# Kernel optimization log

Hardware: AMD Instinct MI355X
Metric: run time of the kernel (lower is better)

Reference implementation:

```python
import jax, jax.numpy as jnp
import numpy as np

B, N, C = 1, 768, 128


def _safe_cdist(x):
    # Euclidean pairwise distance, grad-safe at zero (diagonal).
    sq = jnp.sum(x * x, axis=-1)  # (b, n)
    d2 = sq[:, :, None] + sq[:, None, :] - 2.0 * jnp.einsum('bmi,bni->bmn', x, x)
    d2 = jnp.maximum(d2, 0.0)
    pos = d2 > 0
    return jnp.where(pos, jnp.sqrt(jnp.where(pos, d2, 1.0)), 0.0)


def _bilinear(h, Wa, ba, Wb, bb):
    # Gated bilinear unit: Linear_a(h) * Linear_b(h)
    return (h @ Wa.T + ba) * (h @ Wb.T + bb)


def setup_inputs() -> dict:
    key = jax.random.key(0)
    ks = jax.random.split(key, 16)
    x = jax.random.normal(ks[0], (B, N, 3), dtype=jnp.float32)

    def lin(k, fan_in, fan_out):
        k1, k2 = jax.random.split(k)
        s = 1.0 / np.sqrt(fan_in)
        W = jax.random.uniform(k1, (fan_out, fan_in), jnp.float32, -s, s)
        b = jax.random.uniform(k2, (fan_out,), jnp.float32, -s, s)
        return W, b

    Wa1, ba1 = lin(ks[1], 3, C)
    Wb1, bb1 = lin(ks[2], 3, C)
    Wa2, ba2 = lin(ks[3], C, C)
    Wb2, bb2 = lin(ks[4], C, C)
    Wa3, ba3 = lin(ks[5], C, C)
    Wb3, bb3 = lin(ks[6], C, C)
    Wf, _ = lin(ks[7], C, 2)  # final bias unused by the einsum in forward
    return {"x": x,
            "Wa1": Wa1, "ba1": ba1, "Wb1": Wb1, "bb1": bb1,
            "Wa2": Wa2, "ba2": ba2, "Wb2": Wb2, "bb2": bb2,
            "Wa3": Wa3, "ba3": ba3, "Wb3": Wb3, "bb3": bb3,
            "Wf": Wf}


def reference(x, Wa1, ba1, Wb1, bb1, Wa2, ba2, Wb2, bb2, Wa3, ba3, Wb3, bb3, Wf):
    b, n, _ = x.shape
    nrm = jnp.linalg.norm(x, axis=-1, keepdims=True)          # (b, n, 1)
    nrm_m = jnp.broadcast_to(nrm, (b, n, n))                  # row norms
    d = _safe_cdist(x)                                        # (b, n, n)
    h = jnp.stack([d, nrm_m, jnp.swapaxes(nrm_m, 1, 2)], axis=-1)  # (b,n,n,3)
    h = _bilinear(h, Wa1, ba1, Wb1, bb1)
    h = _bilinear(h, Wa2, ba2, Wb2, bb2)
    h = _bilinear(h, Wa3, ba3, Wb3, bb3)                      # (b,n,n,C)
    att = jax.nn.softmax(h, axis=-2)                          # softmax over n (dim=-2)
    # einsum('bmnc,bni->bmic') followed by sum over m, fused:
    agg = jnp.einsum('bmnc,bni->bic', att, x)                 # (b, 3, C)
    agg = jnp.swapaxes(agg, 1, 2)                             # (b, C, 3)
    out = jnp.einsum('bnd,on->bod', agg, Wf)                  # (b, 2, 3)
    return jnp.concatenate([x[:, :1], out[:, :2]], axis=1)    # (b, 3, 3)
```

## Files before the change

### kernel.cpp

```cpp
#include <hip/hip_runtime.h>

#define NPTS 768
#define CCH  128
#define NM4  36
#define NM2  10
#define TILE 128
#define NCHUNK 6
#define PAIR (NPTS*CCH)
#define NACC 384
#define FINB 96
#define LOG2E 1.4426950408889634f
#define NQW  (NPTS*8*CCH)

typedef __attribute__((ext_vector_type(8))) short bf16x8;
typedef __attribute__((ext_vector_type(16))) float f32x16;
union Frag { unsigned int u[4]; bf16x8 h; };

__device__ __forceinline__ float fast_exp2(float x) {
  return __builtin_amdgcn_exp2f(x);
}

__device__ __forceinline__ void split3(float x, unsigned int& h0,
                                       unsigned int& h1, unsigned int& h2) {
  const unsigned int b0 = __float_as_uint(x);
  h0 = b0 >> 16;
  const float r1 = x - __uint_as_float(b0 & 0xFFFF0000u);
  const unsigned int b1 = __float_as_uint(r1);
  h1 = b1 >> 16;
  const float r2 = r1 - __uint_as_float(b1 & 0xFFFF0000u);
  h2 = __float_as_uint(r2) >> 16;
}

__device__ __forceinline__ int t4i(int a, int b, int c) {
  int t = 0;
  for (int aa = 0; aa < a; ++aa) t += (5 - aa) * (6 - aa) / 2;
  for (int bb = 0; bb < b; ++bb) t += (5 - a - bb);
  return t + c;
}
__device__ __forceinline__ int t2i(int a, int b, int c) {
  int t = 0;
  for (int aa = 0; aa < a; ++aa) t += (3 - aa) * (4 - aa) / 2;
  for (int bb = 0; bb < b; ++bb) t += (3 - a - bb);
  return t + c;
}

__global__ __launch_bounds__(128) void k_fold12(
    const float* __restrict__ x,
    const float* __restrict__ Wa1, const float* __restrict__ ba1,
    const float* __restrict__ Wb1, const float* __restrict__ bb1,
    const float* __restrict__ Wa2, const float* __restrict__ ba2,
    const float* __restrict__ Wb2, const float* __restrict__ bb2,
    float* __restrict__ norms, float* __restrict__ C2m,
    float* __restrict__ apart, unsigned int* __restrict__ ticket) {
  __shared__ float sA[128][NM2];
  __shared__ float sB[128][NM2];
  const int c = blockIdx.x;
  const int k = threadIdx.x;

  if (c < 6) {
    const int i = c*128 + k;
    const float p0 = x[3*i], p1 = x[3*i+1], p2 = x[3*i+2];
    norms[i] = sqrtf(p0*p0 + p1*p1 + p2*p2);
  }
  if (c == 6) {
    apart[k] = 0.f; apart[CCH + k] = 0.f; apart[2*CCH + k] = 0.f;
    if (k == 0) *ticket = 0u;
  }

  {
    const float A0 = Wa1[3*k], A1 = Wa1[3*k+1], A2c = Wa1[3*k+2], A3 = ba1[k];
    const float B0 = Wb1[3*k], B1 = Wb1[3*k+1], B2c = Wb1[3*k+2], B3 = bb1[k];
    const float g0 = A3*B3;
    const float g1 = A2c*B3 + A3*B2c;
    const float g2 = A2c*B2c;
    const float g3 = A1*B3 + A3*B1;
    const float g4 = A1*B2c + A2c*B1;
    const float g5 = A1*B1;
    const float g6 = A0*B3 + A3*B0;
    const float g7 = A0*B2c + A2c*B0;
    const float g8 = A0*B1 + A1*B0;
    const float g9 = A0*B0;
    const float wa = Wa2[c*CCH + k];
    const float wb = Wb2[c*CCH + k];
    sA[k][0] = wa*g0; sB[k][0] = wb*g0;
    sA[k][1] = wa*g1; sB[k][1] = wb*g1;
    sA[k][2] = wa*g2; sB[k][2] = wb*g2;
    sA[k][3] = wa*g3; sB[k][3] = wb*g3;
    sA[k][4] = wa*g4; sB[k][4] = wb*g4;
    sA[k][5] = wa*g5; sB[k][5] = wb*g5;
    sA[k][6] = wa*g6; sB[k][6] = wb*g6;
    sA[k][7] = wa*g7; sB[k][7] = wb*g7;
    sA[k][8] = wa*g8; sB[k][8] = wb*g8;
    sA[k][9] = wa*g9; sB[k][9] = wb*g9;
  }
  __syncthreads();

  for (int s = 64; s >= 1; s >>= 1) {
    if (k < s) {
      for (int t = 0; t < NM2; ++t) {
        sA[k][t] += sA[k+s][t];
        sB[k][t] += sB[k+s][t];
      }
    }
    __syncthreads();
  }
  if (k == 0) {
    sA[0][0] += ba2[c];
    sB[0][0] += bb2[c];
  }
  __syncthreads();

  if (k < 35) {
    int rem = k, a = 0;
    while (rem >= (5 - a)*(6 - a)/2) { rem -= (5 - a)*(6 - a)/2; ++a; }
    int b = 0;
    while (rem >= 5 - a - b) { rem -= 5 - a - b; ++b; }
    const int cc = rem;
    float s = 0.f;
    const int deg = a + b + cc;
    for (int a1 = 0; a1 <= a && a1 <= 2; ++a1)
      for (int b1 = 0; b1 <= b && b1 <= 2; ++b1)
        for (int c1 = 0; c1 <= cc && c1 <= 2; ++c1) {
          const int d1 = a1 + b1 + c1;
          if (d1 <= 2 && (deg - d1) <= 2)
            s += sA[0][t2i(a1, b1, c1)]
               * sB[0][t2i(a - a1, b - b1, cc - c1)];
        }
    C2m[c*NM4 + k] = s;
  }
  if (k == 35) C2m[c*NM4 + 35] = 0.f;
}

__global__ void k_pre2(const float* __restrict__ Wa3, const float* __restrict__ ba3,
                       const float* __restrict__ Wb3, const float* __restrict__ bb3,
                       const float* __restrict__ C2m,
                       float* __restrict__ A3mT, float* __restrict__ B3mT) {
  const int c = blockIdx.x;
  const int j = threadIdx.x;
  if (j >= NM4) return;
  float sa = 0.f, sb = 0.f;
  if (j < 35) {
    for (int k = 0; k < CCH; ++k) {
      const float v = C2m[k*NM4 + j];
      sa += Wa3[c*CCH + k] * v;
      sb += Wb3[c*CCH + k] * v;
    }
    if (j == 0) { sa += ba3[c]; sb += bb3[c]; }
  }
  A3mT[j*CCH + c] = sa;
  B3mT[j*CCH + c] = sb;
}

__global__ __launch_bounds__(256) void k_pre3(
    const float* __restrict__ norms,
    const float* __restrict__ A3mT, const float* __restrict__ B3mT,
    unsigned int* __restrict__ WA0, unsigned int* __restrict__ WA1,
    unsigned int* __restrict__ WA2, unsigned int* __restrict__ WB0,
    unsigned int* __restrict__ WB1, unsigned int* __restrict__ WB2) {
  const int m = blockIdx.x;
  const float u = norms[m];
  float upow[5];
  upow[0] = 1.f; upow[1] = u; upow[2] = u*u;
  upow[3] = upow[2]*u; upow[4] = upow[2]*upow[2];

  for (int p = threadIdx.x; p < 8*CCH; p += 256) {
    const int q = p >> 7;
    const int c = p & 127;
    unsigned int wa0 = 0, wa1 = 0, wa2 = 0, wb0 = 0, wb1 = 0, wb2 = 0;
    #pragma unroll
    for (int half = 0; half < 2; ++half) {
      const int t = 2*q + half;
      int rem = t, i = 0;
      while (i < 5 && rem >= 5 - i) { rem -= 5 - i; ++i; }
      const int j = rem;
      float sa = 0.f, sb = 0.f;
      #pragma unroll
      for (int b = 0; b < 5; ++b) {
        if (i <= 4 && i + j + b <= 4) {
          const int idx = t4i(i, b, j)*CCH + c;
          sa = fmaf(A3mT[idx], upow[b], sa);
          sb = fmaf(B3mT[idx], upow[b], sb);
        }
      }
      sa *= LOG2E;
      unsigned int a0, a1, a2, b0, b1, b2;
      split3(sa, a0, a1, a2);
      split3(sb, b0, b1, b2);
      const int sh = half*16;
      wa0 |= a0 << sh; wa1 |= a1 << sh; wa2 |= a2 << sh;
      wb0 |= b0 << sh; wb1 |= b1 << sh; wb2 |= b2 << sh;
    }
    const int o = (m*8 + q)*CCH + c;
    WA0[o] = wa0; WA1[o] = wa1; WA2[o] = wa2;
    WB0[o] = wb0; WB1[o] = wb1; WB2[o] = wb2;
  }
}

__global__ __launch_bounds__(256, 2) void k_main(
    const float* __restrict__ x, const float* __restrict__ norms,
    const unsigned int* __restrict__ WA0, const unsigned int* __restrict__ WA1,
    const unsigned int* __restrict__ WA2, const unsigned int* __restrict__ WB0,
    const unsigned int* __restrict__ WB1, const unsigned int* __restrict__ WB2,
    float* __restrict__ Mp, float* __restrict__ Sp,
    float* __restrict__ A0p, float* __restrict__ A1p, float* __restrict__ A2p) {
  __shared__ __align__(16) float4 xt[TILE];
  const int tid = threadIdx.x;
  const int wid = tid >> 6;
  const int lane = tid & 63;
  const int hl = lane >> 5;
  const int ln = lane & 31;
  const int m = blockIdx.x*4 + wid;
  const int chunk = blockIdx.y;

  if (tid < TILE) {
    const int n = chunk*TILE + tid;
    xt[tid] = make_float4(x[3*n], x[3*n+1], x[3*n+2], norms[n]);
  }

  const float u = norms[m];
  const float xm0 = x[3*m], xm1 = x[3*m+1], xm2 = x[3*m+2];
  const float uu = u*u;

  Frag BA0[4], BA1[4], BA2[4], BB0[4], BB1[4], BB2[4];
  #pragma unroll
  for (int ct = 0; ct < 4; ++ct) {
    #pragma unroll
    for (int p = 0; p < 4; ++p) {
      const int o = (m*8 + hl*4 + p)*CCH + ct*32 + ln;
      BA0[ct].u[p] = WA0[o]; BA1[ct].u[p] = WA1[o]; BA2[ct].u[p] = WA2[o];
      BB0[ct].u[p] = WB0[o]; BB1[ct].u[p] = WB1[o]; BB2[ct].u[p] = WB2[o];
    }
  }

  float mrun[4], srun[4], a0r[4], a1r[4], a2r[4];
  #pragma unroll
  for (int ct = 0; ct < 4; ++ct) {
    mrun[ct] = -INFINITY; srun[ct] = 0.f;
    a0r[ct] = 0.f; a1r[ct] = 0.f; a2r[ct] = 0.f;
  }

  __syncthreads();

  for (int tile = 0; tile < 4; ++tile) {
    const float4 xn = xt[tile*32 + ln];
    const float v = xn.w;
    const float dot = xm0*xn.x + xm1*xn.y + xm2*xn.z;
    const float d2 = uu + v*v - 2.f*dot;
    const float d = (d2 > 0.f) ? sqrtf(d2) : 0.f;
    const float v2 = v*v, v3 = v2*v, v4 = v2*v2;
    const float dd = d*d, d3 = dd*d, d4 = dd*dd;
    float mono[8];
    if (hl == 0) {
      mono[0] = 1.f;   mono[1] = v;     mono[2] = v2;    mono[3] = v3;
      mono[4] = v4;    mono[5] = d;     mono[6] = d*v;   mono[7] = d*v2;
    } else {
      mono[0] = d*v3;  mono[1] = dd;    mono[2] = dd*v;  mono[3] = dd*v2;
      mono[4] = d3;    mono[5] = d3*v;  mono[6] = d4;    mono[7] = 0.f;
    }
    Frag A0f, A1f, A2f;
    #pragma unroll
    for (int p = 0; p < 4; ++p) {
      unsigned int l0, l1, l2, g0, g1, g2;
      split3(mono[2*p],   l0, l1, l2);
      split3(mono[2*p+1], g0, g1, g2);
      A0f.u[p] = l0 | (g0 << 16);
      A1f.u[p] = l1 | (g1 << 16);
      A2f.u[p] = l2 | (g2 << 16);
    }

    #pragma unroll
    for (int ct = 0; ct < 4; ++ct) {
      f32x16 accA, accB;
      #pragma unroll
      for (int r = 0; r < 16; ++r) { accA[r] = 0.f; accB[r] = 0.f; }
      accA = __builtin_amdgcn_mfma_f32_32x32x16_bf16(A2f.h, BA0[ct].h, accA, 0, 0, 0);
      accA = __builtin_amdgcn_mfma_f32_32x32x16_bf16(A1f.h, BA1[ct].h, accA, 0, 0, 0);
      accA = __builtin_amdgcn_mfma_f32_32x32x16_bf16(A0f.h, BA2[ct].h, accA, 0, 0, 0);
      accA = __builtin_amdgcn_mfma_f32_32x32x16_bf16(A1f.h, BA0[ct].h, accA, 0, 0, 0);
      accA = __builtin_amdgcn_mfma_f32_32x32x16_bf16(A0f.h, BA1[ct].h, accA, 0, 0, 0);
      accA = __builtin_amdgcn_mfma_f32_32x32x16_bf16(A0f.h, BA0[ct].h, accA, 0, 0, 0);
      accB = __builtin_amdgcn_mfma_f32_32x32x16_bf16(A2f.h, BB0[ct].h, accB, 0, 0, 0);
      accB = __builtin_amdgcn_mfma_f32_32x32x16_bf16(A1f.h, BB1[ct].h, accB, 0, 0, 0);
      accB = __builtin_amdgcn_mfma_f32_32x32x16_bf16(A0f.h, BB2[ct].h, accB, 0, 0, 0);
      accB = __builtin_amdgcn_mfma_f32_32x32x16_bf16(A1f.h, BB0[ct].h, accB, 0, 0, 0);
      accB = __builtin_amdgcn_mfma_f32_32x32x16_bf16(A0f.h, BB1[ct].h, accB, 0, 0, 0);
      accB = __builtin_amdgcn_mfma_f32_32x32x16_bf16(A0f.h, BB0[ct].h, accB, 0, 0, 0);

      float hv[16];
      #pragma unroll
      for (int r = 0; r < 16; ++r) hv[r] = accA[r]*accB[r];
      float hx = hv[0];
      #pragma unroll
      for (int r = 1; r < 16; ++r) hx = fmaxf(hx, hv[r]);
      const float mnew = fmaxf(mrun[ct], hx);
      const float sc = fast_exp2(mrun[ct] - mnew);
      mrun[ct] = mnew;
      float s_ = srun[ct]*sc, A0_ = a0r[ct]*sc, A1_ = a1r[ct]*sc, A2_ = a2r[ct]*sc;
      #pragma unroll
      for (int rg = 0; rg < 4; ++rg) {
        #pragma unroll
        for (int q = 0; q < 4; ++q) {
          const float e = fast_exp2(hv[rg*4 + q] - mnew);
          const float4 xv = xt[tile*32 + rg*8 + hl*4 + q];
          s_ += e;
          A0_ = fmaf(e, xv.x, A0_);
          A1_ = fmaf(e, xv.y, A1_);
          A2_ = fmaf(e, xv.z, A2_);
        }
      }
      srun[ct] = s_; a0r[ct] = A0_; a1r[ct] = A1_; a2r[ct] = A2_;
    }
  }

  #pragma unroll
  for (int ct = 0; ct < 4; ++ct) {
    const float om = __shfl_xor(mrun[ct], 32);
    const float os = __shfl_xor(srun[ct], 32);
    const float o0 = __shfl_xor(a0r[ct], 32);
    const float o1 = __shfl_xor(a1r[ct], 32);
    const float o2 = __shfl_xor(a2r[ct], 32);
    const float M  = fmaxf(mrun[ct], om);
    const float e1 = fast_exp2(mrun[ct] - M);
    const float e2 = fast_exp2(om - M);
    if (hl == 0) {
      const int idx = chunk*PAIR + m*CCH + ct*32 + ln;
      Mp[idx]  = M;
      Sp[idx]  = fmaf(srun[ct], e1, os*e2);
      A0p[idx] = fmaf(a0r[ct], e1, o0*e2);
      A1p[idx] = fmaf(a1r[ct], e1, o1*e2);
      A2p[idx] = fmaf(a2r[ct], e1, o2*e2);
    }
  }
}

__global__ __launch_bounds__(256) void k_fin(
    const float* __restrict__ x,
    const float* __restrict__ Mp, const float* __restrict__ Sp,
    const float* __restrict__ A0p, const float* __restrict__ A1p,
    const float* __restrict__ A2p,
    const float* __restrict__ Wf,
    float* __restrict__ apart, unsigned int* __restrict__ ticket,
    float* __restrict__ out) {
  __shared__ float red2[2][3][CCH];
  __shared__ float red[CCH][6];
  __shared__ bool last;
  const int tid = threadIdx.x;
  const int ml = tid >> 7;
  const int c = tid & 127;

  float s0 = 0.f, s1 = 0.f, s2 = 0.f;
  #pragma unroll
  for (int j = 0; j < 4; ++j) {
    const int m = blockIdx.x*8 + ml*4 + j;
    const int gid = m*CCH + c;
    float m0 = Mp[0*PAIR + gid], m1 = Mp[1*PAIR + gid], m2 = Mp[2*PAIR + gid];
    float m3 = Mp[3*PAIR + gid], m4 = Mp[4*PAIR + gid], m5 = Mp[5*PAIR + gid];
    float M = fmaxf(fmaxf(fmaxf(m0, m1), fmaxf(m2, m3)), fmaxf(m4, m5));
    float W = 0.f, g0 = 0.f, g1 = 0.f, g2 = 0.f;
    {
      const float e0 = fast_exp2(m0 - M), e1 = fast_exp2(m1 - M);
      const float e2 = fast_exp2(m2 - M), e3 = fast_exp2(m3 - M);
      const float e4 = fast_exp2(m4 - M), e5 = fast_exp2(m5 - M);
      W = Sp[0*PAIR+gid]*e0 + Sp[1*PAIR+gid]*e1 + Sp[2*PAIR+gid]*e2
        + Sp[3*PAIR+gid]*e3 + Sp[4*PAIR+gid]*e4 + Sp[5*PAIR+gid]*e5;
      g0 = A0p[0*PAIR+gid]*e0 + A0p[1*PAIR+gid]*e1 + A0p[2*PAIR+gid]*e2
         + A0p[3*PAIR+gid]*e3 + A0p[4*PAIR+gid]*e4 + A0p[5*PAIR+gid]*e5;
      g1 = A1p[0*PAIR+gid]*e0 + A1p[1*PAIR+gid]*e1 + A1p[2*PAIR+gid]*e2
         + A1p[3*PAIR+gid]*e3 + A1p[4*PAIR+gid]*e4 + A1p[5*PAIR+gid]*e5;
      g2 = A2p[0*PAIR+gid]*e0 + A2p[1*PAIR+gid]*e1 + A2p[2*PAIR+gid]*e2
         + A2p[3*PAIR+gid]*e3 + A2p[4*PAIR+gid]*e4 + A2p[5*PAIR+gid]*e5;
    }
    const float inv = 1.f / W;
    s0 = fmaf(g0, inv, s0);
    s1 = fmaf(g1, inv, s1);
    s2 = fmaf(g2, inv, s2);
  }
  red2[ml][0][c] = s0; red2[ml][1][c] = s1; red2[ml][2][c] = s2;
  __syncthreads();
  for (int p = tid; p < NACC; p += 256) {
    const int i = p >> 7, cc = p & 127;
    atomicAdd(&apart[p], red2[0][i][cc] + red2[1][i][cc]);
  }
  __threadfence();
  __syncthreads();
  if (tid == 0) {
    const unsigned int old = atomicAdd(ticket, 1u);
    last = (old == FINB - 1);
  }
  __syncthreads();
  if (!last) return;
  __threadfence();

  if (tid < CCH) {
    const int cc = tid;
    const float a0 = __hip_atomic_load(&apart[cc],          __ATOMIC_RELAXED, __HIP_MEMORY_SCOPE_AGENT);
    const float a1 = __hip_atomic_load(&apart[CCH + cc],    __ATOMIC_RELAXED, __HIP_MEMORY_SCOPE_AGENT);
    const float a2 = __hip_atomic_load(&apart[2*CCH + cc],  __ATOMIC_RELAXED, __HIP_MEMORY_SCOPE_AGENT);
    const float w0 = Wf[cc], w1 = Wf[CCH + cc];
    red[cc][0] = w0*a0; red[cc][1] = w0*a1; red[cc][2] = w0*a2;
    red[cc][3] = w1*a0; red[cc][4] = w1*a1; red[cc][5] = w1*a2;
  }
  __syncthreads();
  if (tid < 6) {
    float s = 0.f;
    for (int k = 0; k < CCH; ++k) s += red[k][tid];
    out[3 + tid] = s;
  }
  if (tid < 3) out[tid] = x[tid];
}

extern "C" void kernel_launch(void* const* d_in, const int* in_sizes, int n_in,
                              void* d_out, int out_size, void* d_ws, size_t ws_size,
                              hipStream_t stream) {
  const float* x   = (const float*)d_in[0];
  const float* Wa1 = (const float*)d_in[1];
  const float* ba1 = (const float*)d_in[2];
  const float* Wb1 = (const float*)d_in[3];
  const float* bb1 = (const float*)d_in[4];
  const float* Wa2 = (const float*)d_in[5];
  const float* ba2 = (const float*)d_in[6];
  const float* Wb2 = (const float*)d_in[7];
  const float* bb2 = (const float*)d_in[8];
  const float* Wa3 = (const float*)d_in[9];
  const float* ba3 = (const float*)d_in[10];
  const float* Wb3 = (const float*)d_in[11];
  const float* bb3 = (const float*)d_in[12];
  const float* Wf  = (const float*)d_in[13];
  float* out = (float*)d_out;

  float* ws     = (float*)d_ws;
  float* norms  = ws;
  float* C2m    = norms + NPTS;
  float* A3mT   = C2m   + CCH*NM4;
  float* B3mT   = A3mT  + NM4*CCH;
  float* Mp     = B3mT  + NM4*CCH;
  float* Sp     = Mp    + NCHUNK*PAIR;
  float* A0p    = Sp    + NCHUNK*PAIR;
  float* A1p    = A0p   + NCHUNK*PAIR;
  float* A2p    = A1p   + NCHUNK*PAIR;
  float* apart  = A2p   + NCHUNK*PAIR;
  unsigned int* ticket = (unsigned int*)(apart + NACC);

  size_t off = (((size_t)((char*)(ticket + 1) - (char*)d_ws)) + 255) & ~(size_t)255;
  unsigned int* WA0 = (unsigned int*)((char*)d_ws + off);
  unsigned int* WA1 = WA0 + NQW;
  unsigned int* WA2 = WA1 + NQW;
  unsigned int* WB0 = WA2 + NQW;
  unsigned int* WB1 = WB0 + NQW;
  unsigned int* WB2 = WB1 + NQW;

  hipLaunchKernelGGL(k_fold12, dim3(CCH), dim3(128), 0, stream,
                     x, Wa1, ba1, Wb1, bb1, Wa2, ba2, Wb2, bb2,
                     norms, C2m, apart, ticket);
  hipLaunchKernelGGL(k_pre2, dim3(CCH), dim3(64), 0, stream,
                     Wa3, ba3, Wb3, bb3, C2m, A3mT, B3mT);
  hipLaunchKernelGGL(k_pre3, dim3(NPTS), dim3(256), 0, stream,
                     norms, A3mT, B3mT, WA0, WA1, WA2, WB0, WB1, WB2);
  hipLaunchKernelGGL(k_main, dim3(NPTS/4, NCHUNK), dim3(256), 0, stream,
                     x, norms, WA0, WA1, WA2, WB0, WB1, WB2,
                     Mp, Sp, A0p, A1p, A2p);
  hipLaunchKernelGGL(k_fin, dim3(FINB), dim3(256), 0, stream,
                     x, Mp, Sp, A0p, A1p, A2p, Wf, apart, ticket, out);
}
```

Measured before the change: 172.2 us.

## Fuse per-row weight precompute into main kernel and remap channels to waves

Removes the k_pre3 kernel and the large global workspace of split-bf16 per-row weight fragments. Each block now handles one row m, and each wave computes its own 32-channel slice of the polynomial-in-u weights directly from A3mT/B3mT in registers. The column split drops from 6 chunks to 2, so each block sweeps 384 columns and k_fin merges only two partials. The cost is recomputing the weight fold in every block (grid 768x2), redundant per-chunk recompute, and a higher occupancy target through launch bounds.

Result: faster. 155.7 us (-9.6%).

```diff
diff --git a/kernel.cpp b/kernel.cpp
--- a/kernel.cpp
+++ b/kernel.cpp
@@ -4,13 +4,12 @@
 #define CCH  128
 #define NM4  36
 #define NM2  10
-#define TILE 128
-#define NCHUNK 6
+#define NCHUNK 2
+#define CTILE (NPTS/NCHUNK)
 #define PAIR (NPTS*CCH)
 #define NACC 384
 #define FINB 96
 #define LOG2E 1.4426950408889634f
-#define NQW  (NPTS*8*CCH)
 
 typedef __attribute__((ext_vector_type(8))) short bf16x8;
 typedef __attribute__((ext_vector_type(16))) float f32x16;
@@ -151,35 +150,48 @@
   B3mT[j*CCH + c] = sb;
 }
 
-__global__ __launch_bounds__(256) void k_pre3(
-    const float* __restrict__ norms,
+__global__ __launch_bounds__(256, 4) void k_main(
+    const float* __restrict__ x, const float* __restrict__ norms,
     const float* __restrict__ A3mT, const float* __restrict__ B3mT,
-    unsigned int* __restrict__ WA0, unsigned int* __restrict__ WA1,
-    unsigned int* __restrict__ WA2, unsigned int* __restrict__ WB0,
-    unsigned int* __restrict__ WB1, unsigned int* __restrict__ WB2) {
+    float* __restrict__ Mp, float* __restrict__ Sp,
+    float* __restrict__ A0p, float* __restrict__ A1p, float* __restrict__ A2p) {
+  __shared__ __align__(16) float4 xt[CTILE];
+  const int tid = threadIdx.x;
+  const int wid = tid >> 6;
+  const int lane = tid & 63;
+  const int hl = lane >> 5;
+  const int ln = lane & 31;
   const int m = blockIdx.x;
+  const int chunk = blockIdx.y;
+  const int c = wid*32 + ln;
+
+  for (int p = tid; p < CTILE; p += 256) {
+    const int n = chunk*CTILE + p;
+    xt[p] = make_float4(x[3*n], x[3*n+1], x[3*n+2], norms[n]);
+  }
+
   const float u = norms[m];
-  float upow[5];
-  upow[0] = 1.f; upow[1] = u; upow[2] = u*u;
-  upow[3] = upow[2]*u; upow[4] = upow[2]*upow[2];
-
-  for (int p = threadIdx.x; p < 8*CCH; p += 256) {
-    const int q = p >> 7;
-    const int c = p & 127;
+  const float xm0 = x[3*m], xm1 = x[3*m+1], xm2 = x[3*m+2];
+  const float uu = u*u;
+  const float up[5] = {1.f, u, uu, uu*u, uu*uu};
+
+  Frag ba0, ba1, ba2, bb0, bb1, bb2;
+  #pragma unroll
+  for (int p = 0; p < 4; ++p) {
     unsigned int wa0 = 0, wa1 = 0, wa2 = 0, wb0 = 0, wb1 = 0, wb2 = 0;
     #pragma unroll
     for (int half = 0; half < 2; ++half) {
-      const int t = 2*q + half;
+      const int t = 8*hl + 2*p + half;
       int rem = t, i = 0;
       while (i < 5 && rem >= 5 - i) { rem -= 5 - i; ++i; }
       const int j = rem;
       float sa = 0.f, sb = 0.f;
       #pragma unroll
       for (int b = 0; b < 5; ++b) {
-        if (i <= 4 && i + j + b <= 4) {
+        if (i + j + b <= 4) {
           const int idx = t4i(i, b, j)*CCH + c;
-          sa = fmaf(A3mT[idx], upow[b], sa);
-          sb = fmaf(B3mT[idx], upow[b], sb);
+          sa = fmaf(A3mT[idx], up[b], sa);
+          sb = fmaf(B3mT[idx], up[b], sb);
         }
       }
       sa *= LOG2E;
@@ -190,58 +202,15 @@
       wa0 |= a0 << sh; wa1 |= a1 << sh; wa2 |= a2 << sh;
       wb0 |= b0 << sh; wb1 |= b1 << sh; wb2 |= b2 << sh;
     }
-    const int o = (m*8 + q)*CCH + c;
-    WA0[o] = wa0; WA1[o] = wa1; WA2[o] = wa2;
-    WB0[o] = wb0; WB1[o] = wb1; WB2[o] = wb2;
-  }
-}
-
-__global__ __launch_bounds__(256, 2) void k_main(
-    const float* __restrict__ x, const float* __restrict__ norms,
-    const unsigned int* __restrict__ WA0, const unsigned int* __restrict__ WA1,
-    const unsigned int* __restrict__ WA2, const unsigned int* __restrict__ WB0,
-    const unsigned int* __restrict__ WB1, const unsigned int* __restrict__ WB2,
-    float* __restrict__ Mp, float* __restrict__ Sp,
-    float* __restrict__ A0p, float* __restrict__ A1p, float* __restrict__ A2p) {
-  __shared__ __align__(16) float4 xt[TILE];
-  const int tid = threadIdx.x;
-  const int wid = tid >> 6;
-  const int lane = tid & 63;
-  const int hl = lane >> 5;
-  const int ln = lane & 31;
-  const int m = blockIdx.x*4 + wid;
-  const int chunk = blockIdx.y;
-
-  if (tid < TILE) {
-    const int n = chunk*TILE + tid;
-    xt[tid] = make_float4(x[3*n], x[3*n+1], x[3*n+2], norms[n]);
-  }
-
-  const float u = norms[m];
-  const float xm0 = x[3*m], xm1 = x[3*m+1], xm2 = x[3*m+2];
-  const float uu = u*u;
-
-  Frag BA0[4], BA1[4], BA2[4], BB0[4], BB1[4], BB2[4];
-  #pragma unroll
-  for (int ct = 0; ct < 4; ++ct) {
-    #pragma unroll
-    for (int p = 0; p < 4; ++p) {
-      const int o = (m*8 + hl*4 + p)*CCH + ct*32 + ln;
-      BA0[ct].u[p] = WA0[o]; BA1[ct].u[p] = WA1[o]; BA2[ct].u[p] = WA2[o];
-      BB0[ct].u[p] = WB0[o]; BB1[ct].u[p] = WB1[o]; BB2[ct].u[p] = WB2[o];
-    }
-  }
-
-  float mrun[4], srun[4], a0r[4], a1r[4], a2r[4];
-  #pragma unroll
-  for (int ct = 0; ct < 4; ++ct) {
-    mrun[ct] = -INFINITY; srun[ct] = 0.f;
-    a0r[ct] = 0.f; a1r[ct] = 0.f; a2r[ct] = 0.f;
-  }
-
-  __syncthreads();
-
-  for (int tile = 0; tile < 4; ++tile) {
+    ba0.u[p] = wa0; ba1.u[p] = wa1; ba2.u[p] = wa2;
+    bb0.u[p] = wb0; bb1.u[p] = wb1; bb2.u[p] = wb2;
+  }
+
+  __syncthreads();
+
+  float mrun = -INFINITY, srun = 0.f, a0r = 0.f, a1r = 0.f, a2r = 0.f;
+
+  for (int tile = 0; tile < CTILE/32; ++tile) {
     const float4 xn = xt[tile*32 + ln];
     const float v = xn.w;
     const float dot = xm0*xn.x + xm1*xn.y + xm2*xn.z;
@@ -268,67 +237,63 @@
       A2f.u[p] = l2 | (g2 << 16);
     }
 
-    #pragma unroll
-    for (int ct = 0; ct < 4; ++ct) {
-      f32x16 accA, accB;
+    f32x16 accA, accB;
+    #pragma unroll
+    for (int r = 0; r < 16; ++r) { accA[r] = 0.f; accB[r] = 0.f; }
+    accA = __builtin_amdgcn_mfma_f32_32x32x16_bf16(A2f.h, ba0.h, accA, 0, 0, 0);
+    accA = __builtin_amdgcn_mfma_f32_32x32x16_bf16(A1f.h, ba1.h, accA, 0, 0, 0);
+    accA = __builtin_amdgcn_mfma_f32_32x32x16_bf16(A0f.h, ba2.h, accA, 0, 0, 0);
+    accA = __builtin_amdgcn_mfma_f32_32x32x16_bf16(A1f.h, ba0.h, accA, 0, 0, 0);
+    accA = __builtin_amdgcn_mfma_f32_32x32x16_bf16(A0f.h, ba1.h, accA, 0, 0, 0);
+    accA = __builtin_amdgcn_mfma_f32_32x32x16_bf16(A0f.h, ba0.h, accA, 0, 0, 0);
+    accB = __builtin_amdgcn_mfma_f32_32x32x16_bf16(A2f.h, bb0.h, accB, 0, 0, 0);
+    accB = __builtin_amdgcn_mfma_f32_32x32x16_bf16(A1f.h, bb1.h, accB, 0, 0, 0);
+    accB = __builtin_amdgcn_mfma_f32_32x32x16_bf16(A0f.h, bb2.h, accB, 0, 0, 0);
+    accB = __builtin_amdgcn_mfma_f32_32x32x16_bf16(A1f.h, bb0.h, accB, 0, 0, 0);
+    accB = __builtin_amdgcn_mfma_f32_32x32x16_bf16(A0f.h, bb1.h, accB, 0, 0, 0);
+    accB = __builtin_amdgcn_mfma_f32_32x32x16_bf16(A0f.h, bb0.h, accB, 0, 0, 0);
+
+    float hv[16];
+    #pragma unroll
+    for (int r = 0; r < 16; ++r) hv[r] = accA[r]*accB[r];
+    float hx = hv[0];
+    #pragma unroll
+    for (int r = 1; r < 16; ++r) hx = fmaxf(hx, hv[r]);
+    const float mnew = fmaxf(mrun, hx);
+    const float sc = fast_exp2(mrun - mnew);
+    mrun = mnew;
+    float s_ = srun*sc, A0_ = a0r*sc, A1_ = a1r*sc, A2_ = a2r*sc;
+    #pragma unroll
+    for (int rg = 0; rg < 4; ++rg) {
       #pragma unroll
-      for (int r = 0; r < 16; ++r) { accA[r] = 0.f; accB[r] = 0.f; }
-      accA = __builtin_amdgcn_mfma_f32_32x32x16_bf16(A2f.h, BA0[ct].h, accA, 0, 0, 0);
-      accA = __builtin_amdgcn_mfma_f32_32x32x16_bf16(A1f.h, BA1[ct].h, accA, 0, 0, 0);
-      accA = __builtin_amdgcn_mfma_f32_32x32x16_bf16(A0f.h, BA2[ct].h, accA, 0, 0, 0);
-      accA = __builtin_amdgcn_mfma_f32_32x32x16_bf16(A1f.h, BA0[ct].h, accA, 0, 0, 0);
-      accA = __builtin_amdgcn_mfma_f32_32x32x16_bf16(A0f.h, BA1[ct].h, accA, 0, 0, 0);
-      accA = __builtin_amdgcn_mfma_f32_32x32x16_bf16(A0f.h, BA0[ct].h, accA, 0, 0, 0);
-      accB = __builtin_amdgcn_mfma_f32_32x32x16_bf16(A2f.h, BB0[ct].h, accB, 0, 0, 0);
-      accB = __builtin_amdgcn_mfma_f32_32x32x16_bf16(A1f.h, BB1[ct].h, accB, 0, 0, 0);
-      accB = __builtin_amdgcn_mfma_f32_32x32x16_bf16(A0f.h, BB2[ct].h, accB, 0, 0, 0);
-      accB = __builtin_amdgcn_mfma_f32_32x32x16_bf16(A1f.h, BB0[ct].h, accB, 0, 0, 0);
-      accB = __builtin_amdgcn_mfma_f32_32x32x16_bf16(A0f.h, BB1[ct].h, accB, 0, 0, 0);
-      accB = __builtin_amdgcn_mfma_f32_32x32x16_bf16(A0f.h, BB0[ct].h, accB, 0, 0, 0);
-
-      float hv[16];
-      #pragma unroll
-      for (int r = 0; r < 16; ++r) hv[r] = accA[r]*accB[r];
-      float hx = hv[0];
-      #pragma unroll
-      for (int r = 1; r < 16; ++r) hx = fmaxf(hx, hv[r]);
-      const float mnew = fmaxf(mrun[ct], hx);
-      const float sc = fast_exp2(mrun[ct] - mnew);
-      mrun[ct] = mnew;
-      float s_ = srun[ct]*sc, A0_ = a0r[ct]*sc, A1_ = a1r[ct]*sc, A2_ = a2r[ct]*sc;
-      #pragma unroll
-      for (int rg = 0; rg < 4; ++rg) {
-        #pragma unroll
-        for (int q = 0; q < 4; ++q) {
-          const float e = fast_exp2(hv[rg*4 + q] - mnew);
-          const float4 xv = xt[tile*32 + rg*8 + hl*4 + q];
-          s_ += e;
-          A0_ = fmaf(e, xv.x, A0_);
-          A1_ = fmaf(e, xv.y, A1_);
-          A2_ = fmaf(e, xv.z, A2_);
-        }
+      for (int q = 0; q < 4; ++q) {
+        const float e = fast_exp2(hv[rg*4 + q] - mnew);
+        const float4 xv = xt[tile*32 + rg*8 + hl*4 + q];
+        s_ += e;
+        A0_ = fmaf(e, xv.x, A0_);
+        A1_ = fmaf(e, xv.y, A1_);
+        A2_ = fmaf(e, xv.z, A2_);
       }
-      srun[ct] = s_; a0r[ct] = A0_; a1r[ct] = A1_; a2r[ct] = A2_;
-    }
-  }
-
-  #pragma unroll
-  for (int ct = 0; ct < 4; ++ct) {
-    const float om = __shfl_xor(mrun[ct], 32);
-    const float os = __shfl_xor(srun[ct], 32);
-    const float o0 = __shfl_xor(a0r[ct], 32);
-    const float o1 = __shfl_xor(a1r[ct], 32);
-    const float o2 = __shfl_xor(a2r[ct], 32);
-    const float M  = fmaxf(mrun[ct], om);
-    const float e1 = fast_exp2(mrun[ct] - M);
+    }
+    srun = s_; a0r = A0_; a1r = A1_; a2r = A2_;
+  }
+
+  {
+    const float om = __shfl_xor(mrun, 32);
+    const float os = __shfl_xor(srun, 32);
+    const float o0 = __shfl_xor(a0r, 32);
+    const float o1 = __shfl_xor(a1r, 32);
+    const float o2 = __shfl_xor(a2r, 32);
+    const float M  = fmaxf(mrun, om);
+    const float e1 = fast_exp2(mrun - M);
     const float e2 = fast_exp2(om - M);
     if (hl == 0) {
-      const int idx = chunk*PAIR + m*CCH + ct*32 + ln;
+      const int idx = chunk*PAIR + m*CCH + c;
       Mp[idx]  = M;
-      Sp[idx]  = fmaf(srun[ct], e1, os*e2);
-      A0p[idx] = fmaf(a0r[ct], e1, o0*e2);
-      A1p[idx] = fmaf(a1r[ct], e1, o1*e2);
-      A2p[idx] = fmaf(a2r[ct], e1, o2*e2);
+      Sp[idx]  = fmaf(srun, e1, os*e2);
+      A0p[idx] = fmaf(a0r, e1, o0*e2);
+      A1p[idx] = fmaf(a1r, e1, o1*e2);
+      A2p[idx] = fmaf(a2r, e1, o2*e2);
     }
   }
 }
@@ -353,23 +318,13 @@
   for (int j = 0; j < 4; ++j) {
     const int m = blockIdx.x*8 + ml*4 + j;
     const int gid = m*CCH + c;
-    float m0 = Mp[0*PAIR + gid], m1 = Mp[1*PAIR + gid], m2 = Mp[2*PAIR + gid];
-    float m3 = Mp[3*PAIR + gid], m4 = Mp[4*PAIR + gid], m5 = Mp[5*PAIR + gid];
-    float M = fmaxf(fmaxf(fmaxf(m0, m1), fmaxf(m2, m3)), fmaxf(m4, m5));
-    float W = 0.f, g0 = 0.f, g1 = 0.f, g2 = 0.f;
-    {
-      const float e0 = fast_exp2(m0 - M), e1 = fast_exp2(m1 - M);
-      const float e2 = fast_exp2(m2 - M), e3 = fast_exp2(m3 - M);
-      const float e4 = fast_exp2(m4 - M), e5 = fast_exp2(m5 - M);
-      W = Sp[0*PAIR+gid]*e0 + Sp[1*PAIR+gid]*e1 + Sp[2*PAIR+gid]*e2
-        + Sp[3*PAIR+gid]*e3 + Sp[4*PAIR+gid]*e4 + Sp[5*PAIR+gid]*e5;
-      g0 = A0p[0*PAIR+gid]*e0 + A0p[1*PAIR+gid]*e1 + A0p[2*PAIR+gid]*e2
-         + A0p[3*PAIR+gid]*e3 + A0p[4*PAIR+gid]*e4 + A0p[5*PAIR+gid]*e5;
-      g1 = A1p[0*PAIR+gid]*e0 + A1p[1*PAIR+gid]*e1 + A1p[2*PAIR+gid]*e2
-         + A1p[3*PAIR+gid]*e3 + A1p[4*PAIR+gid]*e4 + A1p[5*PAIR+gid]*e5;
-      g2 = A2p[0*PAIR+gid]*e0 + A2p[1*PAIR+gid]*e1 + A2p[2*PAIR+gid]*e2
-         + A2p[3*PAIR+gid]*e3 + A2p[4*PAIR+gid]*e4 + A2p[5*PAIR+gid]*e5;
-    }
+    const float m0 = Mp[0*PAIR + gid], m1 = Mp[1*PAIR + gid];
+    const float M = fmaxf(m0, m1);
+    const float e0 = fast_exp2(m0 - M), e1 = fast_exp2(m1 - M);
+    const float W  = Sp[0*PAIR+gid]*e0 + Sp[1*PAIR+gid]*e1;
+    const float g0 = A0p[0*PAIR+gid]*e0 + A0p[1*PAIR+gid]*e1;
+    const float g1 = A1p[0*PAIR+gid]*e0 + A1p[1*PAIR+gid]*e1;
+    const float g2 = A2p[0*PAIR+gid]*e0 + A2p[1*PAIR+gid]*e1;
     const float inv = 1.f / W;
     s0 = fmaf(g0, inv, s0);
     s1 = fmaf(g1, inv, s1);
@@ -441,24 +396,13 @@
   float* apart  = A2p   + NCHUNK*PAIR;
   unsigned int* ticket = (unsigned int*)(apart + NACC);
 
-  size_t off = (((size_t)((char*)(ticket + 1) - (char*)d_ws)) + 255) & ~(size_t)255;
-  unsigned int* WA0 = (unsigned int*)((char*)d_ws + off);
-  unsigned int* WA1 = WA0 + NQW;
-  unsigned int* WA2 = WA1 + NQW;
-  unsigned int* WB0 = WA2 + NQW;
-  unsigned int* WB1 = WB0 + NQW;
-  unsigned int* WB2 = WB1 + NQW;
-
   hipLaunchKernelGGL(k_fold12, dim3(CCH), dim3(128), 0, stream,
                      x, Wa1, ba1, Wb1, bb1, Wa2, ba2, Wb2, bb2,
                      norms, C2m, apart, ticket);
   hipLaunchKernelGGL(k_pre2, dim3(CCH), dim3(64), 0, stream,
                      Wa3, ba3, Wb3, bb3, C2m, A3mT, B3mT);
-  hipLaunchKernelGGL(k_pre3, dim3(NPTS), dim3(256), 0, stream,
-                     norms, A3mT, B3mT, WA0, WA1, WA2, WB0, WB1, WB2);
-  hipLaunchKernelGGL(k_main, dim3(NPTS/4, NCHUNK), dim3(256), 0, stream,
-                     x, norms, WA0, WA1, WA2, WB0, WB1, WB2,
-                     Mp, Sp, A0p, A1p, A2p);
+  hipLaunchKernelGGL(k_main, dim3(NPTS, NCHUNK), dim3(256), 0, stream,
+                     x, norms, A3mT, B3mT, Mp, Sp, A0p, A1p, A2p);
   hipLaunchKernelGGL(k_fin, dim3(FINB), dim3(256), 0, stream,
                      x, Mp, Sp, A0p, A1p, A2p, Wf, apart, ticket, out);
 }
```
